# Optimization experiments

Hardware: AMD Instinct MI355X
Metric: run time of the kernel (lower is better)

Reference implementation:

```python
import jax, jax.numpy as jnp
import numpy as np

B, C, H, W = 16, 64, 1024, 16  # requires C*W == H per the module's implicit view/matmul constraint
C8 = C // 8


def setup_inputs() -> dict:
    key = jax.random.key(0)
    ks = jax.random.split(key, 7)
    s_in = 1.0 / np.sqrt(C)
    return {
        "x": jax.random.normal(ks[0], (B, C, H, W), dtype=jnp.float32),
        "Wq": jax.random.normal(ks[1], (C8, C), dtype=jnp.float32) * s_in,
        "bq": jax.random.normal(ks[2], (C8,), dtype=jnp.float32) * 0.01,
        "Wk": jax.random.normal(ks[3], (C8, C), dtype=jnp.float32) * s_in,
        "bk": jax.random.normal(ks[4], (C8,), dtype=jnp.float32) * 0.01,
        "Wv": jax.random.normal(ks[5], (C, C), dtype=jnp.float32) * s_in,
        "bv": jax.random.normal(ks[6], (C,), dtype=jnp.float32) * 0.01,
    }


def conv1x1(x, w, b):
    # 1x1 conv == per-pixel channel mixing: [B,C,H,W] x [O,C] -> [B,O,H,W]
    return jnp.einsum("bchw,oc->bohw", x, w) + b[None, :, None, None]


def reference(x, Wq, bq, Wk, bk, Wv, bv):
    b, c, h, w = x.shape
    q = conv1x1(x, Wq, bq)  # [B, C/8, H, W]
    k = conv1x1(x, Wk, bk)  # [B, C/8, H, W]
    v = conv1x1(x, Wv, bv)  # [B, C, H, W]
    # Faithful to torch .view(B, -1, H): row-major reshape, NOT a transpose.
    qf = jnp.swapaxes(q.reshape(b, -1, h), 1, 2)  # [B, H, C8*W]
    kf = k.reshape(b, -1, h)                      # [B, C8*W, H]
    vf = v.reshape(b, -1, h)                      # [B, C*W, H] (C*W == H)
    scores = jax.nn.softmax(jnp.matmul(qf, kf), axis=-1)  # [B, H, H]
    attended = jnp.matmul(scores, vf)             # [B, H, H]
    attended = attended.reshape(v.shape)          # [B, C, H, W]
    return x + attended
```

## Files before the change

### kernel.cpp

```cpp
#include <hip/hip_runtime.h>
#include <stdint.h>

typedef uint32_t u32;
typedef __attribute__((ext_vector_type(4))) float f32x4;
typedef __attribute__((ext_vector_type(8))) short short8;

#define NBATCH 16
#define NPIX   16384
#define NPB    1048576

__device__ __forceinline__ ushort f2bf(float f) {
  u32 b = __builtin_bit_cast(u32, f);
  return (ushort)((b + 0x7FFFu + ((b >> 16) & 1u)) >> 16);
}
__device__ __forceinline__ float bf2f(ushort h) {
  return __builtin_bit_cast(float, (u32)h << 16);
}

__device__ __forceinline__ void gload16(const void* g, void* l) {
  __builtin_amdgcn_global_load_lds(
      (const __attribute__((address_space(1))) u32*)g,
      (__attribute__((address_space(3))) u32*)l,
      16, 0, 0);
}

__global__ void prep_w2(const float* __restrict__ Wq, const float* __restrict__ bq,
                        const float* __restrict__ Wk, const float* __restrict__ bk,
                        const float* __restrict__ Wv, const float* __restrict__ bv,
                        ushort* __restrict__ Wpk, float* __restrict__ bpk)
{
  int gid = blockIdx.x * 256 + threadIdx.x;
  if (gid < 12288) {
    int m = gid >> 7, kk = gid & 127;
    int ch = kk & 63;
    ushort outv = 0;
    if (m < 8) {
      float wv = Wq[m * 64 + ch];
      ushort h = f2bf(wv);
      outv = (kk < 64) ? h : f2bf(wv - bf2f(h));
    } else if (m < 16) {
      float wv = Wk[(m - 8) * 64 + ch];
      ushort h = f2bf(wv);
      outv = (kk < 64) ? h : f2bf(wv - bf2f(h));
    } else if (m < 80) {
      outv = (kk < 64) ? f2bf(Wv[(m - 16) * 64 + ch]) : (ushort)0;
    }
    Wpk[gid] = outv;
  } else if (gid < 12368) {
    int o = gid - 12288;
    bpk[o] = (o < 8) ? bq[o] : (o < 16 ? bk[o - 8] : bv[o - 16]);
  }
}

__global__ __launch_bounds__(256) void proj12(
    const float* __restrict__ x, const ushort* __restrict__ Wpk,
    const float* __restrict__ bpk,
    ushort* __restrict__ Qt2, ushort* __restrict__ Kt2,
    ushort* __restrict__ Vt)
{
  __shared__ __align__(16) char smem[65536];
  int t = threadIdx.x;
  int w = t >> 6, lane = t & 63;
  int l15 = lane & 15, l4 = lane >> 4;

  int g = blockIdx.x;
  int lin = (g & 7) * 128 + (g >> 3);
  int b = lin >> 6;
  int l0 = (lin & 63) << 4;

  const uint4* Wp4 = (const uint4*)Wpk;
  uint4 Afrag[12];
  #pragma unroll
  for (int kc = 0; kc < 4; ++kc)
    Afrag[kc] = Wp4[l15 * 16 + kc * 4 + l4];
  #pragma unroll
  for (int mt = 1; mt < 5; ++mt)
    #pragma unroll
    for (int kc = 0; kc < 2; ++kc)
      Afrag[2 + mt * 2 + kc] = Wp4[(mt * 16 + l15) * 16 + kc * 4 + l4];
  __builtin_amdgcn_sched_barrier(0);

  #pragma unroll
  for (int c = 0; c < 2; ++c) {
    const float* xb = x + (size_t)b * NPB + l0 + c * 8;
    float* xs = (float*)(smem + c * 32768);
    #pragma unroll
    for (int it = 0; it < 8; ++it) {
      int f0 = (it * 4 + w) * 64;
      int f = f0 + lane;
      int ch = f >> 5, r2 = f & 31, tc = r2 >> 1, half = r2 & 1;
      gload16(xb + (size_t)ch * NPIX + tc * 1024 + half * 4, xs + f0 * 4);
    }
  }
  asm volatile("s_waitcnt vmcnt(8)" ::: "memory");
  __builtin_amdgcn_sched_barrier(0);
  __builtin_amdgcn_s_barrier();

  auto do_chunk = [&](char* region, int lc) {
    float* xs = (float*)region;
    f32x4 acc[5][2];
    #pragma unroll
    for (int mt = 0; mt < 5; ++mt) {
      f32x4 bv4;
      #pragma unroll
      for (int r = 0; r < 4; ++r) bv4[r] = bpk[mt * 16 + l4 * 4 + r];
      acc[mt][0] = bv4; acc[mt][1] = bv4;
    }
    #pragma unroll
    for (int i = 0; i < 2; ++i) {
      int px = (w * 2 + i) * 16 + l15;
      u32 xr[16];
      #pragma unroll
      for (int kc = 0; kc < 2; ++kc)
        #pragma unroll
        for (int j = 0; j < 8; ++j)
          xr[kc * 8 + j] = ((const u32*)xs)[(kc * 32 + l4 * 8 + j) * 128 + px];
      uint4 bxh[2], bxl[2];
      #pragma unroll
      for (int kc = 0; kc < 2; ++kc)
        #pragma unroll
        for (int p = 0; p < 4; ++p) {
          u32 a = xr[kc * 8 + 2 * p], cc = xr[kc * 8 + 2 * p + 1];
          ((u32*)&bxh[kc])[p] = (a >> 16) | (cc & 0xFFFF0000u);
          float fa = __builtin_bit_cast(float, a) -
                     __builtin_bit_cast(float, a & 0xFFFF0000u);
          float fc = __builtin_bit_cast(float, cc) -
                     __builtin_bit_cast(float, cc & 0xFFFF0000u);
          u32 la = __builtin_bit_cast(u32, fa), lc2 = __builtin_bit_cast(u32, fc);
          ((u32*)&bxl[kc])[p] = (la >> 16) | (lc2 & 0xFFFF0000u);
        }
      short8 h0 = __builtin_bit_cast(short8, bxh[0]);
      short8 h1 = __builtin_bit_cast(short8, bxh[1]);
      short8 s0 = __builtin_bit_cast(short8, bxl[0]);
      short8 s1 = __builtin_bit_cast(short8, bxl[1]);
      acc[0][i] = __builtin_amdgcn_mfma_f32_16x16x32_bf16(
          __builtin_bit_cast(short8, Afrag[0]), h0, acc[0][i], 0, 0, 0);
      acc[0][i] = __builtin_amdgcn_mfma_f32_16x16x32_bf16(
          __builtin_bit_cast(short8, Afrag[1]), h1, acc[0][i], 0, 0, 0);
      acc[0][i] = __builtin_amdgcn_mfma_f32_16x16x32_bf16(
          __builtin_bit_cast(short8, Afrag[0]), s0, acc[0][i], 0, 0, 0);
      acc[0][i] = __builtin_amdgcn_mfma_f32_16x16x32_bf16(
          __builtin_bit_cast(short8, Afrag[1]), s1, acc[0][i], 0, 0, 0);
      acc[0][i] = __builtin_amdgcn_mfma_f32_16x16x32_bf16(
          __builtin_bit_cast(short8, Afrag[2]), h0, acc[0][i], 0, 0, 0);
      acc[0][i] = __builtin_amdgcn_mfma_f32_16x16x32_bf16(
          __builtin_bit_cast(short8, Afrag[3]), h1, acc[0][i], 0, 0, 0);
      #pragma unroll
      for (int mt = 1; mt < 5; ++mt) {
        acc[mt][i] = __builtin_amdgcn_mfma_f32_16x16x32_bf16(
            __builtin_bit_cast(short8, Afrag[2 + mt * 2]), h0, acc[mt][i], 0, 0, 0);
        acc[mt][i] = __builtin_amdgcn_mfma_f32_16x16x32_bf16(
            __builtin_bit_cast(short8, Afrag[3 + mt * 2]), h1, acc[mt][i], 0, 0, 0);
      }
    }
    __syncthreads();

    float*  qkl = (float*)region;
    ushort* vl  = (ushort*)(region + 16 * 132 * 4);
    #pragma unroll
    for (int i = 0; i < 2; ++i) {
      int px = (w * 2 + i) * 16 + l15;
      #pragma unroll
      for (int r = 0; r < 4; ++r)
        qkl[(l4 * 4 + r) * 132 + px] = acc[0][i][r];
      #pragma unroll
      for (int mt = 1; mt < 5; ++mt)
        #pragma unroll
        for (int r = 0; r < 4; ++r)
          vl[((mt - 1) * 16 + l4 * 4 + r) * 136 + px] = f2bf(acc[mt][i][r]);
    }
    __syncthreads();

    if (t < 128) {
      int l = t >> 4, tcc = t & 15;
      size_t lrow = (size_t)b * 1024 + lc + l;
      int px = tcc * 8 + l;

      union { ushort s[8]; uint4 v; } qh, ql, kh, kl;
      #pragma unroll
      for (int o = 0; o < 8; ++o) {
        float qv = qkl[o * 132 + px];
        ushort h = f2bf(qv);
        qh.s[o] = h; ql.s[o] = f2bf(qv - bf2f(h));
        float kv = qkl[(8 + o) * 132 + px];
        h = f2bf(kv);
        kh.s[o] = h; kl.s[o] = f2bf(kv - bf2f(h));
      }
      ushort* qrow = Qt2 + lrow * 256 + tcc * 8;
      *(uint4*)qrow         = qh.v;
      *(uint4*)(qrow + 128) = ql.v;
      ushort* krow = Kt2 + lrow * 256 + tcc * 8;
      *(uint4*)krow         = kh.v;
      *(uint4*)(krow + 128) = kl.v;

      ushort* vrow = Vt + lrow * 1024;
      #pragma unroll
      for (int it = 0; it < 4; ++it) {
        int c2 = (it << 4) + tcc;
        union { ushort s[16]; uint4 q[2]; } ov;
        #pragma unroll
        for (int tt = 0; tt < 16; ++tt)
          ov.s[tt] = vl[c2 * 136 + tt * 8 + l];
        *(uint4*)(vrow + c2 * 16)     = ov.q[0];
        *(uint4*)(vrow + c2 * 16 + 8) = ov.q[1];
      }
    }
  };

  do_chunk(smem, l0);
  do_chunk(smem + 32768, l0 + 8);
}

__global__ __launch_bounds__(512, 2) void gemm_qk(
    const ushort* __restrict__ A,
    const ushort* __restrict__ B,
    float* __restrict__ C)
{
  __shared__ ushort AB[2][2][16384];
  int t = threadIdx.x;

  int g = blockIdx.x;
  int lin = (g & 7) * 32 + (g >> 3);
  int bz = lin >> 4;
  int by = (lin >> 2) & 3;
  int bx = lin & 3;
  int m0 = by << 8, n0 = bx << 8;

  const ushort* Ab = A + (size_t)bz * 1024 * 256;
  const ushort* Bb = B + (size_t)bz * 1024 * 256;
  int w = t >> 6, lane = t & 63;
  int wm = w >> 2, wn = w & 3;
  int l15 = lane & 15, l4 = lane >> 4;

  int swc = (t & 7) ^ ((t >> 3) & 7);
  const ushort* pa = Ab + (size_t)(m0 + (t >> 3)) * 256 + swc * 8;
  const ushort* pb = Bb + (size_t)(n0 + (t >> 3)) * 256 + swc * 8;
  int wb = w * 512;

  constexpr int KA[6] = {0, 64, 128, 192, 0, 64};
  constexpr int KB[6] = {0, 64, 0, 64, 128, 192};

  f32x4 acc[8][4] = {};

  #pragma unroll
  for (int i = 0; i < 4; ++i)
    gload16(pa + (size_t)i * 64 * 256 + KA[0], AB[0][0] + i * 4096 + wb);
  #pragma unroll
  for (int i = 0; i < 4; ++i)
    gload16(pb + (size_t)i * 64 * 256 + KB[0], AB[0][1] + i * 4096 + wb);
  #pragma unroll
  for (int i = 0; i < 4; ++i)
    gload16(pa + (size_t)i * 64 * 256 + KA[1], AB[1][0] + i * 4096 + wb);
  #pragma unroll
  for (int i = 0; i < 4; ++i)
    gload16(pb + (size_t)i * 64 * 256 + KB[1], AB[1][1] + i * 4096 + wb);

  for (int it = 0; it < 6; ++it) {
    int cur = it & 1;
    asm volatile("s_waitcnt vmcnt(8)" ::: "memory");
    __builtin_amdgcn_sched_barrier(0);
    __builtin_amdgcn_s_barrier();

    const ushort* As = AB[cur][0];
    const ushort* Bs = AB[cur][1];
    #pragma unroll
    for (int kk = 0; kk < 2; ++kk) {
      short8 af[8], bfr[4];
      #pragma unroll
      for (int mi = 0; mi < 8; ++mi) {
        int rr = (wm << 7) + (mi << 4) + l15;
        af[mi] = __builtin_bit_cast(short8,
            ((const uint4*)As)[rr * 8 + ((kk * 4 + l4) ^ (rr & 7))]);
      }
      #pragma unroll
      for (int ni = 0; ni < 4; ++ni) {
        int rr = (wn << 6) + (ni << 4) + l15;
        bfr[ni] = __builtin_bit_cast(short8,
            ((const uint4*)Bs)[rr * 8 + ((kk * 4 + l4) ^ (rr & 7))]);
      }
      #pragma unroll
      for (int mi = 0; mi < 8; ++mi)
        #pragma unroll
        for (int ni = 0; ni < 4; ++ni)
          acc[mi][ni] = __builtin_amdgcn_mfma_f32_16x16x32_bf16(
              af[mi], bfr[ni], acc[mi][ni], 0, 0, 0);
    }

    asm volatile("" ::: "memory");
    __builtin_amdgcn_s_barrier();
    __builtin_amdgcn_sched_barrier(0);
    if (it + 2 < 6) {
      ushort* An = AB[cur][0];
      ushort* Bn = AB[cur][1];
      #pragma unroll
      for (int i = 0; i < 4; ++i)
        gload16(pa + (size_t)i * 64 * 256 + KA[it + 2], An + i * 4096 + wb);
      #pragma unroll
      for (int i = 0; i < 4; ++i)
        gload16(pb + (size_t)i * 64 * 256 + KB[it + 2], Bn + i * 4096 + wb);
    }
  }

  #pragma unroll
  for (int mi = 0; mi < 8; ++mi) {
    int rbase = m0 + (wm << 7) + (mi << 4) + (l4 << 2);
    #pragma unroll
    for (int ni = 0; ni < 4; ++ni) {
      int col = n0 + (wn << 6) + (ni << 4) + l15;
      f32x4 v = acc[mi][ni];
      #pragma unroll
      for (int rr = 0; rr < 4; ++rr) {
        size_t idx = ((size_t)bz * 1024 + rbase + rr) * 1024 + col;
        C[idx] = v[rr];
      }
    }
  }
}

template<int KTOT, bool ADDX>
__global__ __launch_bounds__(512, 2) void gemm256(
    const ushort* __restrict__ A, int lda,
    const ushort* __restrict__ B, int ldb,
    float* __restrict__ C, const float* __restrict__ X)
{
  __shared__ ushort AB[2][2][16384];
  int t = threadIdx.x;

  int g = blockIdx.x;
  int lin = (g & 7) * 32 + (g >> 3);
  int bz = lin >> 4;
  int by = (lin >> 2) & 3;
  int bx = lin & 3;
  int m0 = by << 8, n0 = bx << 8;

  const ushort* Ab = A + (size_t)bz * 1024 * lda;
  const ushort* Bb = B + (size_t)bz * 1024 * ldb;
  int w = t >> 6, lane = t & 63;
  int wm = w >> 2, wn = w & 3;
  int l15 = lane & 15, l4 = lane >> 4;

  int swc = (t & 7) ^ ((t >> 3) & 7);
  const ushort* pa = Ab + (size_t)(m0 + (t >> 3)) * lda + swc * 8;
  const ushort* pb = Bb + (size_t)(n0 + (t >> 3)) * ldb + swc * 8;
  int wb = w * 512;

  f32x4 acc[8][4] = {};
  constexpr int NT = KTOT / 64;

  #pragma unroll
  for (int i = 0; i < 4; ++i)
    gload16(pa + (size_t)i * 64 * lda, AB[0][0] + i * 4096 + wb);
  #pragma unroll
  for (int i = 0; i < 4; ++i)
    gload16(pb + (size_t)i * 64 * ldb, AB[0][1] + i * 4096 + wb);
  #pragma unroll
  for (int i = 0; i < 4; ++i)
    gload16(pa + (size_t)i * 64 * lda + 64, AB[1][0] + i * 4096 + wb);
  #pragma unroll
  for (int i = 0; i < 4; ++i)
    gload16(pb + (size_t)i * 64 * ldb + 64, AB[1][1] + i * 4096 + wb);

  for (int it = 0; it < NT; ++it) {
    int cur = it & 1;
    asm volatile("s_waitcnt vmcnt(8)" ::: "memory");
    __builtin_amdgcn_sched_barrier(0);
    __builtin_amdgcn_s_barrier();

    const ushort* As = AB[cur][0];
    const ushort* Bs = AB[cur][1];
    #pragma unroll
    for (int kk = 0; kk < 2; ++kk) {
      short8 af[8], bfr[4];
      #pragma unroll
      for (int mi = 0; mi < 8; ++mi) {
        int rr = (wm << 7) + (mi << 4) + l15;
        af[mi] = __builtin_bit_cast(short8,
            ((const uint4*)As)[rr * 8 + ((kk * 4 + l4) ^ (rr & 7))]);
      }
      #pragma unroll
      for (int ni = 0; ni < 4; ++ni) {
        int rr = (wn << 6) + (ni << 4) + l15;
        bfr[ni] = __builtin_bit_cast(short8,
            ((const uint4*)Bs)[rr * 8 + ((kk * 4 + l4) ^ (rr & 7))]);
      }
      #pragma unroll
      for (int mi = 0; mi < 8; ++mi)
        #pragma unroll
        for (int ni = 0; ni < 4; ++ni)
          acc[mi][ni] = __builtin_amdgcn_mfma_f32_16x16x32_bf16(
              af[mi], bfr[ni], acc[mi][ni], 0, 0, 0);
    }

    asm volatile("" ::: "memory");
    __builtin_amdgcn_s_barrier();
    __builtin_amdgcn_sched_barrier(0);
    if (it + 2 < NT) {
      int k0 = (it + 2) * 64;
      ushort* An = AB[cur][0];
      ushort* Bn = AB[cur][1];
      #pragma unroll
      for (int i = 0; i < 4; ++i)
        gload16(pa + (size_t)i * 64 * lda + k0, An + i * 4096 + wb);
      #pragma unroll
      for (int i = 0; i < 4; ++i)
        gload16(pb + (size_t)i * 64 * ldb + k0, Bn + i * 4096 + wb);
    }
  }

  #pragma unroll
  for (int mi = 0; mi < 8; ++mi) {
    int rbase = m0 + (wm << 7) + (mi << 4) + (l4 << 2);
    #pragma unroll
    for (int ni = 0; ni < 4; ++ni) {
      int col = n0 + (wn << 6) + (ni << 4) + l15;
      f32x4 v = acc[mi][ni];
      #pragma unroll
      for (int rr = 0; rr < 4; ++rr) {
        size_t idx = ((size_t)bz * 1024 + rbase + rr) * 1024 + col;
        if (ADDX) C[idx] = v[rr] + X[idx];
        else      C[idx] = v[rr];
      }
    }
  }
}

__global__ __launch_bounds__(256) void softmax_rows(float* __restrict__ S)
{
  size_t rowi = blockIdx.x;
  float* srow = S + rowi * 1024;
  int t = threadIdx.x;
  float4 v = ((const float4*)srow)[t];
  float m = fmaxf(fmaxf(v.x, v.y), fmaxf(v.z, v.w));
  #pragma unroll
  for (int off = 32; off > 0; off >>= 1) m = fmaxf(m, __shfl_xor(m, off));
  __shared__ float red[8];
  int wid = t >> 6, lane = t & 63;
  if (lane == 0) red[wid] = m;
  __syncthreads();
  m = fmaxf(fmaxf(red[0], red[1]), fmaxf(red[2], red[3]));
  float e0 = __expf(v.x - m), e1 = __expf(v.y - m);
  float e2 = __expf(v.z - m), e3 = __expf(v.w - m);
  float s = e0 + e1 + e2 + e3;
  #pragma unroll
  for (int off = 32; off > 0; off >>= 1) s += __shfl_xor(s, off);
  if (lane == 0) red[4 + wid] = s;
  __syncthreads();
  s = red[4] + red[5] + red[6] + red[7];
  float inv = 1.0f / s;
  union { ushort h[4]; uint2 q; } pk;
  pk.h[0] = f2bf(e0 * inv); pk.h[1] = f2bf(e1 * inv);
  pk.h[2] = f2bf(e2 * inv); pk.h[3] = f2bf(e3 * inv);
  ((uint2*)srow)[t] = pk.q;
}

extern "C" void kernel_launch(void* const* d_in, const int* in_sizes, int n_in,
                              void* d_out, int out_size, void* d_ws, size_t ws_size,
                              hipStream_t stream) {
  const float* x  = (const float*)d_in[0];
  const float* Wq = (const float*)d_in[1];
  const float* bq = (const float*)d_in[2];
  const float* Wk = (const float*)d_in[3];
  const float* bk = (const float*)d_in[4];
  const float* Wv = (const float*)d_in[5];
  const float* bv = (const float*)d_in[6];
  float* out = (float*)d_out;

  char* wsb = (char*)d_ws;
  ushort* Qt2 = (ushort*)wsb;
  ushort* Kt2 = (ushort*)(wsb + 8388608);
  ushort* Vt  = (ushort*)(wsb + 16777216);
  float*  S   = (float*)(wsb + 50331648);
  ushort* Wpk = (ushort*)(wsb + 117440512);
  float*  bpk = (float*)(wsb + 117440512 + 24576);

  prep_w2<<<49, 256, 0, stream>>>(Wq, bq, Wk, bk, Wv, bv, Wpk, bpk);
  proj12<<<1024, 256, 0, stream>>>(x, Wpk, bpk, Qt2, Kt2, Vt);
  gemm_qk<<<256, 512, 0, stream>>>(Qt2, Kt2, S);
  softmax_rows<<<16384, 256, 0, stream>>>(S);
  gemm256<1024, true><<<256, 512, 0, stream>>>((const ushort*)S, 2048, Vt, 1024, out, x);
}
```

Baseline: 124.0 us.

## Shrink PV GEMM tile to 128x256 with single-buffered LDS and more blocks

Replaces the double-buffered 256x256 PV GEMM with a 128x256 tile and a single-buffered LDS loop that syncs twice per k-step. The grid grows from 256 to 512 blocks, which should fill more CUs, and launch bounds now allow 4 blocks per CU to recover latency hiding through occupancy. The cost is losing the explicit prefetch overlap and rereading B twice as often across blocks.

```diff
diff --git a/kernel.cpp b/kernel.cpp
--- a/kernel.cpp
+++ b/kernel.cpp
@@ -317,21 +317,22 @@
   }
 }
 
-template<int KTOT, bool ADDX>
-__global__ __launch_bounds__(512, 2) void gemm256(
+__global__ __launch_bounds__(512, 4) void gemm_pv(
     const ushort* __restrict__ A, int lda,
     const ushort* __restrict__ B, int ldb,
     float* __restrict__ C, const float* __restrict__ X)
 {
-  __shared__ ushort AB[2][2][16384];
+  __shared__ ushort Asm[8192];
+  __shared__ ushort Bsm[16384];
   int t = threadIdx.x;
 
   int g = blockIdx.x;
-  int lin = (g & 7) * 32 + (g >> 3);
-  int bz = lin >> 4;
-  int by = (lin >> 2) & 3;
-  int bx = lin & 3;
-  int m0 = by << 8, n0 = bx << 8;
+  int lin = (g & 7) * 64 + (g >> 3);
+  int bz = lin >> 5;
+  int r5 = lin & 31;
+  int by = r5 >> 2;
+  int bx = r5 & 3;
+  int m0 = by << 7, n0 = bx << 8;
 
   const ushort* Ab = A + (size_t)bz * 1024 * lda;
   const ushort* Bb = B + (size_t)bz * 1024 * ldb;
@@ -344,72 +345,46 @@
   const ushort* pb = Bb + (size_t)(n0 + (t >> 3)) * ldb + swc * 8;
   int wb = w * 512;
 
-  f32x4 acc[8][4] = {};
-  constexpr int NT = KTOT / 64;
-
-  #pragma unroll
-  for (int i = 0; i < 4; ++i)
-    gload16(pa + (size_t)i * 64 * lda, AB[0][0] + i * 4096 + wb);
-  #pragma unroll
-  for (int i = 0; i < 4; ++i)
-    gload16(pb + (size_t)i * 64 * ldb, AB[0][1] + i * 4096 + wb);
-  #pragma unroll
-  for (int i = 0; i < 4; ++i)
-    gload16(pa + (size_t)i * 64 * lda + 64, AB[1][0] + i * 4096 + wb);
-  #pragma unroll
-  for (int i = 0; i < 4; ++i)
-    gload16(pb + (size_t)i * 64 * ldb + 64, AB[1][1] + i * 4096 + wb);
-
-  for (int it = 0; it < NT; ++it) {
-    int cur = it & 1;
-    asm volatile("s_waitcnt vmcnt(8)" ::: "memory");
-    __builtin_amdgcn_sched_barrier(0);
-    __builtin_amdgcn_s_barrier();
-
-    const ushort* As = AB[cur][0];
-    const ushort* Bs = AB[cur][1];
+  f32x4 acc[4][4] = {};
+
+  for (int it = 0; it < 16; ++it) {
+    int k0 = it * 64;
+    #pragma unroll
+    for (int i = 0; i < 2; ++i)
+      gload16(pa + (size_t)i * 64 * lda + k0, Asm + i * 4096 + wb);
+    #pragma unroll
+    for (int i = 0; i < 4; ++i)
+      gload16(pb + (size_t)i * 64 * ldb + k0, Bsm + i * 4096 + wb);
+    __syncthreads();
+
     #pragma unroll
     for (int kk = 0; kk < 2; ++kk) {
-      short8 af[8], bfr[4];
-      #pragma unroll
-      for (int mi = 0; mi < 8; ++mi) {
-        int rr = (wm << 7) + (mi << 4) + l15;
+      short8 af[4], bfr[4];
+      #pragma unroll
+      for (int mi = 0; mi < 4; ++mi) {
+        int rr = (wm << 6) + (mi << 4) + l15;
         af[mi] = __builtin_bit_cast(short8,
-            ((const uint4*)As)[rr * 8 + ((kk * 4 + l4) ^ (rr & 7))]);
+            ((const uint4*)Asm)[rr * 8 + ((kk * 4 + l4) ^ (rr & 7))]);
       }
       #pragma unroll
       for (int ni = 0; ni < 4; ++ni) {
         int rr = (wn << 6) + (ni << 4) + l15;
         bfr[ni] = __builtin_bit_cast(short8,
-            ((const uint4*)Bs)[rr * 8 + ((kk * 4 + l4) ^ (rr & 7))]);
-      }
-      #pragma unroll
-      for (int mi = 0; mi < 8; ++mi)
+            ((const uint4*)Bsm)[rr * 8 + ((kk * 4 + l4) ^ (rr & 7))]);
+      }
+      #pragma unroll
+      for (int mi = 0; mi < 4; ++mi)
         #pragma unroll
         for (int ni = 0; ni < 4; ++ni)
           acc[mi][ni] = __builtin_amdgcn_mfma_f32_16x16x32_bf16(
               af[mi], bfr[ni], acc[mi][ni], 0, 0, 0);
     }
-
-    asm volatile("" ::: "memory");
-    __builtin_amdgcn_s_barrier();
-    __builtin_amdgcn_sched_barrier(0);
-    if (it + 2 < NT) {
-      int k0 = (it + 2) * 64;
-      ushort* An = AB[cur][0];
-      ushort* Bn = AB[cur][1];
-      #pragma unroll
-      for (int i = 0; i < 4; ++i)
-        gload16(pa + (size_t)i * 64 * lda + k0, An + i * 4096 + wb);
-      #pragma unroll
-      for (int i = 0; i < 4; ++i)
-        gload16(pb + (size_t)i * 64 * ldb + k0, Bn + i * 4096 + wb);
-    }
-  }
-
-  #pragma unroll
-  for (int mi = 0; mi < 8; ++mi) {
-    int rbase = m0 + (wm << 7) + (mi << 4) + (l4 << 2);
+    __syncthreads();
+  }
+
+  #pragma unroll
+  for (int mi = 0; mi < 4; ++mi) {
+    int rbase = m0 + (wm << 6) + (mi << 4) + (l4 << 2);
     #pragma unroll
     for (int ni = 0; ni < 4; ++ni) {
       int col = n0 + (wn << 6) + (ni << 4) + l15;
@@ -417,8 +392,7 @@
       #pragma unroll
       for (int rr = 0; rr < 4; ++rr) {
         size_t idx = ((size_t)bz * 1024 + rbase + rr) * 1024 + col;
-        if (ADDX) C[idx] = v[rr] + X[idx];
-        else      C[idx] = v[rr];
+        C[idx] = v[rr] + X[idx];
       }
     }
   }
@@ -477,5 +451,5 @@
   proj12<<<1024, 256, 0, stream>>>(x, Wpk, bpk, Qt2, Kt2, Vt);
   gemm_qk<<<256, 512, 0, stream>>>(Qt2, Kt2, S);
   softmax_rows<<<16384, 256, 0, stream>>>(S);
-  gemm256<1024, true><<<256, 512, 0, stream>>>((const ushort*)S, 2048, Vt, 1024, out, x);
-}
+  gemm_pv<<<512, 512, 0, stream>>>((const ushort*)S, 2048, Vt, 1024, out, x);
+}
```

Result: slower. 126.9 us (+2.4%).
